# Performance work log

Measured on AMD Instinct MI355X. Metric: run time of the kernel, lower is better.

The kernel has to match this reference:

```python
import jax, jax.numpy as jnp
import numpy as np

B, L, H, NH, E, M, P, NL, BLK = 4, 1024, 768, 12, 24, 4, 552, 97, 64
NEG = -1e30

def setup_inputs() -> dict:
    key = jax.random.key(0)
    ks = jax.random.split(key, 10)
    sequence_output = jax.random.normal(ks[0], (B, L, H), jnp.float32)
    attention = jax.nn.softmax(jax.random.normal(ks[1], (B, NH, L, L), jnp.float32), axis=-1)
    mention_idx = jax.random.randint(ks[2], (B, E, M), 0, L)
    # first mention of each entity always valid, rest random (ragged mention counts)
    mention_mask = jnp.concatenate(
        [jnp.ones((B, E, 1), jnp.float32),
         (jax.random.uniform(ks[3], (B, E, M - 1)) > 0.4).astype(jnp.float32)], axis=-1)
    hts = jax.random.randint(ks[4], (B, P, 2), 0, E)
    s = 0.02
    Wh = jax.random.normal(ks[5], (H, 2 * H), jnp.float32) * s
    bh = jnp.zeros((H,), jnp.float32)
    Wt = jax.random.normal(ks[6], (H, 2 * H), jnp.float32) * s
    bt = jnp.zeros((H,), jnp.float32)
    Wb = jax.random.normal(ks[7], (NL, H * BLK), jnp.float32) * s
    bb = jnp.zeros((NL,), jnp.float32)
    return {"sequence_output": sequence_output, "attention": attention,
            "mention_mask": mention_mask, "Wh": Wh, "bh": bh, "Wt": Wt, "bt": bt,
            "Wb": Wb, "bb": bb, "mention_idx": mention_idx, "hts": hts}

def reference(sequence_output, attention, mention_mask, Wh, bh, Wt, bt, Wb, bb, mention_idx, hts):
    bix = jnp.arange(B)[:, None, None]
    # gather mention embeddings: [B,E,M,H]
    m_emb = sequence_output[bix, mention_idx]
    mask = mention_mask[..., None]
    # entity embedding: logsumexp over valid mentions
    entity_embs = jax.nn.logsumexp(jnp.where(mask > 0, m_emb, NEG), axis=2)  # [B,E,H]
    # gather mention attention rows: [B,E,M,NH,L]; mean over valid mentions
    m_att = attention[bix, :, mention_idx]
    denom = jnp.sum(mention_mask, axis=-1)[:, :, None, None]
    entity_atts = jnp.sum(m_att * mask[..., None], axis=2) / denom  # [B,E,NH,L]
    b2 = jnp.arange(B)[:, None]
    hs = entity_embs[b2, hts[..., 0]]   # [B,P,H]
    ts = entity_embs[b2, hts[..., 1]]
    h_att = entity_atts[b2, hts[..., 0]]  # [B,P,NH,L]
    t_att = entity_atts[b2, hts[..., 1]]
    ht_att = (h_att * t_att).mean(axis=2)                     # [B,P,L]
    ht_att = ht_att / (ht_att.sum(-1, keepdims=True) + 1e-5)
    rs = jnp.einsum('bld,brl->brd', sequence_output, ht_att)  # [B,P,H]
    zh = jnp.tanh(jnp.concatenate([hs, rs], -1) @ Wh.T + bh)  # [B,P,H]
    zt = jnp.tanh(jnp.concatenate([ts, rs], -1) @ Wt.T + bt)
    b1 = zh.reshape(B, P, H // BLK, BLK)
    b2_ = zt.reshape(B, P, H // BLK, BLK)
    bl = (b1[..., :, None] * b2_[..., None, :]).reshape(B, P, H * BLK)
    logits = bl @ Wb.T + bb                                   # [B,P,NL]
    return logits
```

## Files before the change

kernel.cpp:

```cpp
#include <hip/hip_runtime.h>
#include <math.h>

#define B_   4
#define L_   1024
#define H_   768
#define NH_  12
#define E_   24
#define M_   4
#define P_   552
#define NL_  97
#define H2_  1536
#define HB_  49152
#define R_   2208
#define NEG_ (-1e30f)

#define RT2_  9
#define PR2_  2304
#define S_    48
#define NTIL_ 7
#define KT_   1536

typedef _Float16 h2   __attribute__((ext_vector_type(2)));
typedef _Float16 f16x8 __attribute__((ext_vector_type(8)));
typedef float    f32x4 __attribute__((ext_vector_type(4)));

__device__ inline uint pkh(float lo, float hi) {
    union { __fp16 v __attribute__((ext_vector_type(2))); uint u; } c;
    c.v = __builtin_amdgcn_cvt_pkrtz(lo, hi);
    return c.u;
}
__device__ inline ushort h_rne(float x) {
    union { _Float16 h; ushort u; } c; c.h = (_Float16)x; return c.u;
}
__device__ inline uint h2_rne(float lo, float hi) {
    return (uint)h_rne(lo) | ((uint)h_rne(hi) << 16);
}

#define PKB_ATT 1152
#define PKB_WB  2688
#define PKB_W   576
#define PKB_SEQ 1536
#define PKB_EMB 96
__global__ void k_pack(const float* __restrict__ att, const float* __restrict__ Wb,
                       const float* __restrict__ Wh, const float* __restrict__ Wt,
                       const float* __restrict__ seq,
                       const int* __restrict__ midx, const float* __restrict__ mmask,
                       _Float16* __restrict__ ea, _Float16* __restrict__ WbP,
                       _Float16* __restrict__ WhP, _Float16* __restrict__ WtP,
                       _Float16* __restrict__ seqP, _Float16* __restrict__ ee) {
    int bid = blockIdx.x;
    if (bid < PKB_ATT) {
        int blk = bid;
        int n  = blk % NH_;
        int be = blk / NH_;
        int b  = be / E_;
        int idx[M_]; float msk[M_]; float denom = 0.f;
#pragma unroll
        for (int m = 0; m < M_; ++m) { idx[m] = midx[be*M_+m]; msk[m] = mmask[be*M_+m]; denom += msk[m]; }
        float inv = 1.f / denom;
        const float* abase = att + (size_t)(b*NH_ + n) * L_ * L_;
        int l4 = threadIdx.x * 4;
        float s0 = 0.f, s1 = 0.f, s2 = 0.f, s3 = 0.f;
#pragma unroll
        for (int m = 0; m < M_; ++m) {
            float4 a = *(const float4*)(abase + idx[m]*L_ + l4);
            s0 += msk[m]*a.x; s1 += msk[m]*a.y; s2 += msk[m]*a.z; s3 += msk[m]*a.w;
        }
        *(uint2*)(ea + (((size_t)(be*NH_ + n)) << 10) + l4) =
            make_uint2(pkh(s0*inv, s1*inv), pkh(s2*inv, s3*inv));
        return;
    }
    if (bid < PKB_ATT + PKB_WB) {
        int t = (bid - PKB_ATT)*256 + threadIdx.x;
        int lane = t & 63;
        int nt   = (t >> 6) % NTIL_;
        int kt   = t / (NTIL_*64);
        int n = nt*16 + (lane & 15);
        int k = kt*32 + ((lane >> 4) << 3);
        uint w[4] = {0u,0u,0u,0u};
        if (n < NL_) {
            const float* src = Wb + (size_t)n*HB_ + k;
#pragma unroll
            for (int e = 0; e < 4; ++e) w[e] = h2_rne(src[2*e], src[2*e+1]);
        }
        *(uint4*)(WbP + (size_t)t*8) = make_uint4(w[0],w[1],w[2],w[3]);
        return;
    }
    if (bid < PKB_ATT + PKB_WB + 2*PKB_W) {
        int seg = bid - PKB_ATT - PKB_WB;
        const float* W = (seg < PKB_W) ? Wh : Wt;
        _Float16*   WP = (seg < PKB_W) ? WhP : WtP;
        int t = (seg % PKB_W)*256 + threadIdx.x;
        int lane = t & 63;
        int nt   = (t >> 6) % 48;
        int kt   = t / (48*64);
        int n = nt*16 + (lane & 15);
        int k = kt*32 + ((lane >> 4) << 3);
        const float* src = W + (size_t)n*H2_ + k;
        uint w[4];
#pragma unroll
        for (int e = 0; e < 4; ++e) w[e] = h2_rne(src[2*e], src[2*e+1]);
        *(uint4*)(WP + (size_t)t*8) = make_uint4(w[0],w[1],w[2],w[3]);
        return;
    }
    if (bid < PKB_ATT + PKB_WB + 2*PKB_W + PKB_SEQ) {
        int t = (bid - PKB_ATT - PKB_WB - 2*PKB_W)*256 + threadIdx.x;
        int lane = t & 63;
        int rest = t >> 6;
        int nt = rest % 48; rest /= 48;
        int kt = rest % 32;
        int b  = rest / 32;
        int n = nt*16 + (lane & 15);
        int k = kt*32 + ((lane >> 4) << 3);
        const float* src = seq + ((size_t)(b*L_ + k))*H_ + n;
        uint w[4];
#pragma unroll
        for (int e = 0; e < 4; ++e) w[e] = h2_rne(src[(2*e)*H_], src[(2*e+1)*H_]);
        *(uint4*)(seqP + (size_t)t*8) = make_uint4(w[0],w[1],w[2],w[3]);
        return;
    }
    int be = bid - (PKB_ATT + PKB_WB + 2*PKB_W + PKB_SEQ);
    int b  = be / E_;
    int idx[M_]; float msk[M_];
#pragma unroll
    for (int m = 0; m < M_; ++m) { idx[m] = midx[be*M_+m]; msk[m] = mmask[be*M_+m]; }
    for (int d = threadIdx.x; d < H_; d += 256) {
        float v[M_]; float mx = NEG_;
#pragma unroll
        for (int m = 0; m < M_; ++m) {
            v[m] = (msk[m] > 0.f) ? seq[(b*L_ + idx[m])*H_ + d] : NEG_;
            mx = fmaxf(mx, v[m]);
        }
        float s = 0.f;
#pragma unroll
        for (int m = 0; m < M_; ++m) s += expf(v[m] - mx);
        ee[be*H_ + d] = (_Float16)(mx + logf(s));
    }
}

__global__ void k_ht_att(const _Float16* __restrict__ ea, const int* __restrict__ hts,
                         _Float16* __restrict__ ht) {
    __shared__ float red[2];
    int bp = blockIdx.x;
    int b  = bp / P_;
    int h = hts[bp*2+0], t = hts[bp*2+1];
    const uint4* eh4 = (const uint4*)(ea + ((size_t)(b*E_ + h)*NH_ << 10));
    const uint4* et4 = (const uint4*)(ea + ((size_t)(b*E_ + t)*NH_ << 10));
    int lp = threadIdx.x;
    float s[8] = {};
#pragma unroll
    for (int n = 0; n < NH_; ++n) {
        union { uint4 u; h2 v[4]; } A, C;
        A.u = eh4[n*128 + lp];
        C.u = et4[n*128 + lp];
#pragma unroll
        for (int q = 0; q < 4; ++q) {
            s[2*q]   += (float)A.v[q][0]*(float)C.v[q][0];
            s[2*q+1] += (float)A.v[q][1]*(float)C.v[q][1];
        }
    }
    float local = 0.f;
#pragma unroll
    for (int q = 0; q < 8; ++q) { s[q] *= (1.f/NH_); local += s[q]; }
#pragma unroll
    for (int o = 32; o > 0; o >>= 1) local += __shfl_down(local, o);
    int wid = threadIdx.x >> 6, lane = threadIdx.x & 63;
    if (lane == 0) red[wid] = local;
    __syncthreads();
    if (threadIdx.x == 0) red[0] = 1.f / (red[0] + red[1] + 1e-5f);
    __syncthreads();
    float inv = red[0];
    *(uint4*)(ht + ((size_t)bp << 10) + lp*8) =
        make_uint4(pkh(s[0]*inv, s[1]*inv), pkh(s[2]*inv, s[3]*inv),
                   pkh(s[4]*inv, s[5]*inv), pkh(s[6]*inv, s[7]*inv));
}

__launch_bounds__(256, 2)
__global__ void k_rs_mfma(const _Float16* __restrict__ ht, const _Float16* __restrict__ seqP,
                          _Float16* __restrict__ rs) {
    __shared__ _Float16 as[128*72];
    int bid = blockIdx.x;
    int xcd = bid & 7, jj0 = bid >> 3;
    int b    = xcd >> 1;
    int tile = (xcd & 1)*30 + jj0;
    int p0   = (tile % 5) * 128;
    int nt0  = (tile / 5) * 4;
    int wave = threadIdx.x >> 6, lane = threadIdx.x & 63;

    const _Float16* srcp[4];
    int ldst[4];
#pragma unroll
    for (int i = 0; i < 4; ++i) {
        int t = threadIdx.x + i*256;
        int row = t >> 3, c8 = (t & 7)*8;
        int p = p0 + row;
        srcp[i] = (p < P_) ? ht + (((size_t)(b*P_ + p)) << 10) + c8 : nullptr;
        ldst[i] = row*72 + c8;
    }
    uint4 st[4];
#pragma unroll
    for (int i = 0; i < 4; ++i)
        st[i] = srcp[i] ? *(const uint4*)(srcp[i]) : make_uint4(0,0,0,0);

    f32x4 acc[2][4] = {};
    const _Float16* wbase = seqP + ((size_t)b*32*48 + nt0)*512 + lane*8;
    int rowbase = wave*32 + (lane & 15);
    int asub = (lane >> 4) << 3;

    for (int kc = 0; kc < 16; ++kc) {
        if (kc) __syncthreads();
#pragma unroll
        for (int i = 0; i < 4; ++i) *(uint4*)(as + ldst[i]) = st[i];
        __syncthreads();
        if (kc + 1 < 16) {
#pragma unroll
            for (int i = 0; i < 4; ++i)
                st[i] = srcp[i] ? *(const uint4*)(srcp[i] + (kc+1)*64) : make_uint4(0,0,0,0);
        }
#pragma unroll
        for (int kk = 0; kk < 2; ++kk) {
            int kt = kc*2 + kk;
            const _Float16* wp = wbase + (size_t)kt*(48*512);
            f16x8 bf[4];
#pragma unroll
            for (int jn = 0; jn < 4; ++jn) bf[jn] = *(const f16x8*)(wp + jn*512);
#pragma unroll
            for (int ms = 0; ms < 2; ++ms) {
                f16x8 af = *(const f16x8*)(as + (rowbase + ms*16)*72 + kk*32 + asub);
#pragma unroll
                for (int jn = 0; jn < 4; ++jn)
                    acc[ms][jn] = __builtin_amdgcn_mfma_f32_16x16x32_f16(af, bf[jn], acc[ms][jn], 0, 0, 0);
            }
        }
    }
    int crow = (lane >> 4) * 4;
    int ccol = lane & 15;
#pragma unroll
    for (int ms = 0; ms < 2; ++ms) {
#pragma unroll
        for (int jn = 0; jn < 4; ++jn) {
            int n = nt0*16 + jn*16 + ccol;
#pragma unroll
            for (int reg = 0; reg < 4; ++reg) {
                int p = p0 + wave*32 + ms*16 + crow + reg;
                if (p < P_) rs[(size_t)(b*P_ + p)*H_ + n] = (_Float16)acc[ms][jn][reg];
            }
        }
    }
}

__launch_bounds__(256, 2)
__global__ void k_z_mfma(const _Float16* __restrict__ ee, const _Float16* __restrict__ rs,
                         const _Float16* __restrict__ WhP, const _Float16* __restrict__ WtP,
                         const float* __restrict__ bh, const float* __restrict__ bt,
                         const int* __restrict__ hts,
                         _Float16* __restrict__ zh, _Float16* __restrict__ zt) {
    __shared__ _Float16 as[128*72];
    int bid = blockIdx.x;
    int xcd = bid & 7, jj0 = bid >> 3;
    int which = xcd >> 2;
    int tile  = (xcd & 3)*54 + jj0;
    int r0  = (tile % 18) * 128;
    int nt0 = (tile / 18) * 4;
    const _Float16* WP   = which ? WtP : WhP;
    const float*    bias = which ? bt  : bh;
    _Float16*       out  = which ? zt  : zh;
    int wave = threadIdx.x >> 6, lane = threadIdx.x & 63;

    const _Float16* srcA[4];
    const _Float16* srcB[4];
    int ldst[4];
#pragma unroll
    for (int i = 0; i < 4; ++i) {
        int t = threadIdx.x + i*256;
        int row = t >> 3, c8 = (t & 7)*8;
        int r = r0 + row;
        if (r < R_) {
            int b = r / P_;
            int eidx = hts[r*2 + which];
            srcA[i] = ee + (size_t)(b*E_ + eidx)*H_ + c8;
            srcB[i] = rs + (size_t)r*H_ + c8;
        } else { srcA[i] = nullptr; srcB[i] = nullptr; }
        ldst[i] = row*72 + c8;
    }
    uint4 st[4];
#pragma unroll
    for (int i = 0; i < 4; ++i)
        st[i] = srcA[i] ? *(const uint4*)(srcA[i]) : make_uint4(0,0,0,0);

    f32x4 acc[2][4] = {};
    const _Float16* wbase = WP + (size_t)nt0*512 + lane*8;
    int rowbase = wave*32 + (lane & 15);
    int asub = (lane >> 4) << 3;

    for (int kc = 0; kc < 24; ++kc) {
        if (kc) __syncthreads();
#pragma unroll
        for (int i = 0; i < 4; ++i) *(uint4*)(as + ldst[i]) = st[i];
        __syncthreads();
        if (kc + 1 < 24) {
            int kn = kc + 1;
#pragma unroll
            for (int i = 0; i < 4; ++i) {
                const _Float16* s = (kn < 12) ? (srcA[i] ? srcA[i] + kn*64 : nullptr)
                                              : (srcB[i] ? srcB[i] + (kn-12)*64 : nullptr);
                st[i] = s ? *(const uint4*)s : make_uint4(0,0,0,0);
            }
        }
#pragma unroll
        for (int kk = 0; kk < 2; ++kk) {
            int kt = kc*2 + kk;
            const _Float16* wp = wbase + (size_t)kt*(48*512);
            f16x8 bf[4];
#pragma unroll
            for (int jn = 0; jn < 4; ++jn) bf[jn] = *(const f16x8*)(wp + jn*512);
#pragma unroll
            for (int ms = 0; ms < 2; ++ms) {
                f16x8 af = *(const f16x8*)(as + (rowbase + ms*16)*72 + kk*32 + asub);
#pragma unroll
                for (int jn = 0; jn < 4; ++jn)
                    acc[ms][jn] = __builtin_amdgcn_mfma_f32_16x16x32_f16(af, bf[jn], acc[ms][jn], 0, 0, 0);
            }
        }
    }
    int crow = (lane >> 4) * 4;
    int ccol = lane & 15;
#pragma unroll
    for (int ms = 0; ms < 2; ++ms) {
#pragma unroll
        for (int jn = 0; jn < 4; ++jn) {
            int n = nt0*16 + jn*16 + ccol;
            float bv = bias[n];
#pragma unroll
            for (int reg = 0; reg < 4; ++reg) {
                int r = r0 + wave*32 + ms*16 + crow + reg;
                if (r < R_) out[(size_t)r*H_ + n] = (_Float16)tanhf(acc[ms][jn][reg] + bv);
            }
        }
    }
}

__launch_bounds__(256, 2)
__global__ void k_logits_mfma(const _Float16* __restrict__ zh, const _Float16* __restrict__ zt,
                              const _Float16* __restrict__ WbP, _Float16* __restrict__ part) {
    __shared__ _Float16 zhs[256*20];
    __shared__ _Float16 zts[256*72];
    int bid = blockIdx.x;
    int xcd = bid & 7, j = bid >> 3;
    int kc  = xcd*6 + j/9;
    int rt  = j % 9;
    int r0  = rt * 256;
    int g64 = (kc >> 2) * 64;
    int a0  = (kc & 3) * 16;

    for (int it = 0; it < 2; ++it) {
        int t = threadIdx.x + it*256;
        int row = t >> 1, i8 = (t & 1)*8;
        int r = r0 + row;
        uint4 w = make_uint4(0,0,0,0);
        if (r < R_) w = *(const uint4*)(zh + (size_t)r*H_ + g64 + a0 + i8);
        *(uint4*)(zhs + row*20 + i8) = w;
    }
    for (int it = 0; it < 8; ++it) {
        int t = threadIdx.x + it*256;
        int row = t >> 3, j8 = (t & 7)*8;
        int r = r0 + row;
        uint4 w = make_uint4(0,0,0,0);
        if (r < R_) w = *(const uint4*)(zt + (size_t)r*H_ + g64 + j8);
        *(uint4*)(zts + row*72 + j8) = w;
    }
    __syncthreads();

    int wave = threadIdx.x >> 6, lane = threadIdx.x & 63;
    int rowA0 = wave*64 + (lane & 15);
    int jsub  = (lane >> 4) * 8;

    f32x4 acc[4][NTIL_] = {};
    const _Float16* wb0 = WbP + (size_t)(kc*32) * (NTIL_*512) + lane*8;

    f16x8 bf[NTIL_];
#pragma unroll
    for (int nt = 0; nt < NTIL_; ++nt) bf[nt] = *(const f16x8*)(wb0 + nt*512);

    for (int ktl = 0; ktl < 32; ++ktl) {
        f16x8 bn[NTIL_];
        if (ktl + 1 < 32) {
            const _Float16* wp = wb0 + (size_t)(ktl+1) * (NTIL_*512);
#pragma unroll
            for (int nt = 0; nt < NTIL_; ++nt) bn[nt] = *(const f16x8*)(wp + nt*512);
        }
        int il = ktl >> 1;
        int jb = (ktl & 1) * 32 + jsub;
#pragma unroll
        for (int ms = 0; ms < 4; ++ms) {
            int row = rowA0 + ms*16;
            _Float16 hv = zhs[row*20 + il];
            h2 hb = {hv, hv};
            union { uint4 u; h2 v[4]; } T;
            T.u = *(const uint4*)(zts + row*72 + jb);
            union { h2 v[4]; f16x8 f; } A;
            A.v[0] = hb * T.v[0];
            A.v[1] = hb * T.v[1];
            A.v[2] = hb * T.v[2];
            A.v[3] = hb * T.v[3];
#pragma unroll
            for (int nt = 0; nt < NTIL_; ++nt)
                acc[ms][nt] = __builtin_amdgcn_mfma_f32_16x16x32_f16(A.f, bf[nt], acc[ms][nt], 0, 0, 0);
        }
        if (ktl + 1 < 32) {
#pragma unroll
            for (int nt = 0; nt < NTIL_; ++nt) bf[nt] = bn[nt];
        }
    }

    int crow0 = wave*64 + (lane >> 4) * 4;
    int ccol  = lane & 15;
#pragma unroll
    for (int ms = 0; ms < 4; ++ms) {
#pragma unroll
        for (int nt = 0; nt < NTIL_; ++nt) {
#pragma unroll
            for (int reg = 0; reg < 4; ++reg) {
                int rp = r0 + crow0 + ms*16 + reg;
                part[((size_t)kc*PR2_ + rp)*112 + nt*16 + ccol] = (_Float16)acc[ms][nt][reg];
            }
        }
    }
}

__global__ void k_logits_reduce(const _Float16* __restrict__ part, const float* __restrict__ bb,
                                float* __restrict__ out) {
    int idx = blockIdx.x*256 + threadIdx.x;
    if (idx >= R_*NL_) return;
    int r = idx / NL_, n = idx - r*NL_;
    float s = bb[n];
#pragma unroll
    for (int kc = 0; kc < S_; ++kc) s += (float)part[((size_t)kc*PR2_ + r)*112 + n];
    out[idx] = s;
}

extern "C" void kernel_launch(void* const* d_in, const int* in_sizes, int n_in,
                              void* d_out, int out_size, void* d_ws, size_t ws_size,
                              hipStream_t stream) {
    const float* seq   = (const float*)d_in[0];
    const float* att   = (const float*)d_in[1];
    const float* mmask = (const float*)d_in[2];
    const float* Wh    = (const float*)d_in[3];
    const float* bh    = (const float*)d_in[4];
    const float* Wt    = (const float*)d_in[5];
    const float* bt    = (const float*)d_in[6];
    const float* Wb    = (const float*)d_in[7];
    const float* bb    = (const float*)d_in[8];
    const int*   midx  = (const int*)d_in[9];
    const int*   hts   = (const int*)d_in[10];
    float* out = (float*)d_out;

    char* base = (char*)d_ws;
    _Float16* WbP  = (_Float16*)base;  base += (size_t)KT_*NTIL_*64*8 * 2;
    _Float16* WhP  = (_Float16*)base;  base += (size_t)48*48*64*8 * 2;
    _Float16* WtP  = (_Float16*)base;  base += (size_t)48*48*64*8 * 2;
    _Float16* seqP = (_Float16*)base;  base += (size_t)B_*32*48*64*8 * 2;
    _Float16* ee   = (_Float16*)base;  base += (size_t)B_*E_*H_ * 2;
    _Float16* ea   = (_Float16*)base;  base += (size_t)B_*E_*NH_*L_ * 2;
    _Float16* ht   = (_Float16*)base;  base += (size_t)R_*L_ * 2;
    _Float16* rs   = (_Float16*)base;  base += (size_t)R_*H_ * 2;
    _Float16* zh   = (_Float16*)base;  base += (size_t)R_*H_ * 2;
    _Float16* zt   = (_Float16*)base;  base += (size_t)R_*H_ * 2;
    _Float16* part = (_Float16*)base;

    k_pack<<<dim3(PKB_ATT + PKB_WB + 2*PKB_W + PKB_SEQ + PKB_EMB), dim3(256), 0, stream>>>(
        att, Wb, Wh, Wt, seq, midx, mmask, ea, WbP, WhP, WtP, seqP, ee);

    k_ht_att<<<dim3(R_), dim3(128), 0, stream>>>(ea, hts, ht);

    k_rs_mfma<<<dim3(240), dim3(256), 0, stream>>>(ht, seqP, rs);

    k_z_mfma<<<dim3(432), dim3(256), 0, stream>>>(ee, rs, WhP, WtP, bh, bt, hts, zh, zt);

    k_logits_mfma  <<<dim3(432), dim3(256), 0, stream>>>(zh, zt, WbP, part);
    k_logits_reduce<<<dim3((R_*NL_ + 255)/256), dim3(256), 0, stream>>>(part, bb, out);
}
```

Measured before the change: 114.6 us.

## Stage weight packing through LDS with coalesced float4 loads; raise MFMA launch bounds

Weight packing for Wb, Wh and Wt now reads 16-row by 512-column fp32 tiles with coalesced float4 loads into shared memory, then emits the MFMA-fragment fp16 layout from LDS. The old version did strided scalar reads per lane. This is meant to cut uncoalesced global traffic in the pack kernel, which has to read the large Wb matrix. It adds a 33KB LDS array to every k_pack block, including the attention and seq branches that never use it, which may lower occupancy there. The launch bounds of the rs and z MFMA kernels are also raised to 4 blocks per CU, which may force register spills.

```diff
diff --git a/kernel.cpp b/kernel.cpp
--- a/kernel.cpp
+++ b/kernel.cpp
@@ -37,10 +37,12 @@
 }
 
 #define PKB_ATT 1152
-#define PKB_WB  2688
-#define PKB_W   576
+#define PKB_WB2 672
+#define PKB_W2  288
 #define PKB_SEQ 1536
 #define PKB_EMB 96
+#define LDSTR   516
+
 __global__ void k_pack(const float* __restrict__ att, const float* __restrict__ Wb,
                        const float* __restrict__ Wh, const float* __restrict__ Wt,
                        const float* __restrict__ seq,
@@ -48,6 +50,7 @@
                        _Float16* __restrict__ ea, _Float16* __restrict__ WbP,
                        _Float16* __restrict__ WhP, _Float16* __restrict__ WtP,
                        _Float16* __restrict__ seqP, _Float16* __restrict__ ee) {
+    __shared__ float lds[16][LDSTR];
     int bid = blockIdx.x;
     if (bid < PKB_ATT) {
         int blk = bid;
@@ -70,41 +73,49 @@
             make_uint2(pkh(s0*inv, s1*inv), pkh(s2*inv, s3*inv));
         return;
     }
-    if (bid < PKB_ATT + PKB_WB) {
-        int t = (bid - PKB_ATT)*256 + threadIdx.x;
-        int lane = t & 63;
-        int nt   = (t >> 6) % NTIL_;
-        int kt   = t / (NTIL_*64);
-        int n = nt*16 + (lane & 15);
-        int k = kt*32 + ((lane >> 4) << 3);
-        uint w[4] = {0u,0u,0u,0u};
-        if (n < NL_) {
-            const float* src = Wb + (size_t)n*HB_ + k;
-#pragma unroll
-            for (int e = 0; e < 4; ++e) w[e] = h2_rne(src[2*e], src[2*e+1]);
-        }
-        *(uint4*)(WbP + (size_t)t*8) = make_uint4(w[0],w[1],w[2],w[3]);
+    if (bid < PKB_ATT + PKB_WB2 + PKB_W2) {
+        int seg = bid - PKB_ATT;
+        const float* W; _Float16* WP; int nt, kb, N16, Nvalid, Kdim;
+        if (seg < PKB_WB2) {
+            W = Wb; WP = WbP; N16 = 7; Nvalid = NL_; Kdim = HB_;
+            nt = seg % 7; kb = seg / 7;
+        } else {
+            int s2 = seg - PKB_WB2;
+            int which = s2 / 144;
+            int s = s2 % 144;
+            W = which ? Wt : Wh; WP = which ? WtP : WhP;
+            N16 = 48; Nvalid = H_; Kdim = H2_;
+            nt = s % 48; kb = s / 48;
+        }
+        int k0 = kb * 512;
+#pragma unroll
+        for (int it = 0; it < 8; ++it) {
+            int f4 = threadIdx.x + it*256;
+            int row = f4 >> 7;
+            int c4  = (f4 & 127) << 2;
+            int n   = nt*16 + row;
+            float4 v = make_float4(0.f,0.f,0.f,0.f);
+            if (n < Nvalid) v = *(const float4*)(W + (size_t)n*Kdim + k0 + c4);
+            *(float4*)&lds[row][c4] = v;
+        }
+        __syncthreads();
+        int kt0 = kb * 16;
+#pragma unroll
+        for (int it = 0; it < 4; ++it) {
+            int fi = threadIdx.x + it*256;
+            int kt_l = fi >> 6, lane = fi & 63;
+            int n_l = lane & 15;
+            int k_l = kt_l*32 + ((lane >> 4) << 3);
+            float4 a = *(const float4*)&lds[n_l][k_l];
+            float4 b = *(const float4*)&lds[n_l][k_l + 4];
+            uint4 w = make_uint4(h2_rne(a.x,a.y), h2_rne(a.z,a.w),
+                                 h2_rne(b.x,b.y), h2_rne(b.z,b.w));
+            *(uint4*)(WP + (((size_t)(kt0 + kt_l)*N16 + nt) << 9) + lane*8) = w;
+        }
         return;
     }
-    if (bid < PKB_ATT + PKB_WB + 2*PKB_W) {
-        int seg = bid - PKB_ATT - PKB_WB;
-        const float* W = (seg < PKB_W) ? Wh : Wt;
-        _Float16*   WP = (seg < PKB_W) ? WhP : WtP;
-        int t = (seg % PKB_W)*256 + threadIdx.x;
-        int lane = t & 63;
-        int nt   = (t >> 6) % 48;
-        int kt   = t / (48*64);
-        int n = nt*16 + (lane & 15);
-        int k = kt*32 + ((lane >> 4) << 3);
-        const float* src = W + (size_t)n*H2_ + k;
-        uint w[4];
-#pragma unroll
-        for (int e = 0; e < 4; ++e) w[e] = h2_rne(src[2*e], src[2*e+1]);
-        *(uint4*)(WP + (size_t)t*8) = make_uint4(w[0],w[1],w[2],w[3]);
-        return;
-    }
-    if (bid < PKB_ATT + PKB_WB + 2*PKB_W + PKB_SEQ) {
-        int t = (bid - PKB_ATT - PKB_WB - 2*PKB_W)*256 + threadIdx.x;
+    if (bid < PKB_ATT + PKB_WB2 + PKB_W2 + PKB_SEQ) {
+        int t = (bid - PKB_ATT - PKB_WB2 - PKB_W2)*256 + threadIdx.x;
         int lane = t & 63;
         int rest = t >> 6;
         int nt = rest % 48; rest /= 48;
@@ -119,7 +130,7 @@
         *(uint4*)(seqP + (size_t)t*8) = make_uint4(w[0],w[1],w[2],w[3]);
         return;
     }
-    int be = bid - (PKB_ATT + PKB_WB + 2*PKB_W + PKB_SEQ);
+    int be = bid - (PKB_ATT + PKB_WB2 + PKB_W2 + PKB_SEQ);
     int b  = be / E_;
     int idx[M_]; float msk[M_];
 #pragma unroll
@@ -175,7 +186,7 @@
                    pkh(s[4]*inv, s[5]*inv), pkh(s[6]*inv, s[7]*inv));
 }
 
-__launch_bounds__(256, 2)
+__launch_bounds__(256, 4)
 __global__ void k_rs_mfma(const _Float16* __restrict__ ht, const _Float16* __restrict__ seqP,
                           _Float16* __restrict__ rs) {
     __shared__ _Float16 as[128*72];
@@ -249,7 +260,7 @@
     }
 }
 
-__launch_bounds__(256, 2)
+__launch_bounds__(256, 4)
 __global__ void k_z_mfma(const _Float16* __restrict__ ee, const _Float16* __restrict__ rs,
                          const _Float16* __restrict__ WhP, const _Float16* __restrict__ WtP,
                          const float* __restrict__ bh, const float* __restrict__ bt,
@@ -468,7 +479,7 @@
     _Float16* zt   = (_Float16*)base;  base += (size_t)R_*H_ * 2;
     _Float16* part = (_Float16*)base;
 
-    k_pack<<<dim3(PKB_ATT + PKB_WB + 2*PKB_W + PKB_SEQ + PKB_EMB), dim3(256), 0, stream>>>(
+    k_pack<<<dim3(PKB_ATT + PKB_WB2 + PKB_W2 + PKB_SEQ + PKB_EMB), dim3(256), 0, stream>>>(
         att, Wb, Wh, Wt, seq, midx, mmask, ea, WbP, WhP, WtP, seqP, ee);
 
     k_ht_att<<<dim3(R_), dim3(128), 0, stream>>>(ea, hts, ht);
```

Result: no change. 115.0 us (+0.3%).

## Fuse head and tail projections in z kernel to share rs tile loads

Applied to the files above, without the earlier changes.

The z-projection kernel now computes both zh and zt in one block. Each block loads the rs half of the concatenated input once and feeds it to both the Wh and Wt MFMA streams, while keeping separate LDS tiles for the head and tail entity embeddings during the first half of K. The launch changes from 432 blocks of 256 threads to 216 blocks of 512, with each wave covering 16 rows instead of 32. This halves the rs global and LDS traffic, at the cost of fewer blocks, more registers per thread, and each wave loading weight fragments from both weight matrices.

```diff
diff --git a/kernel.cpp b/kernel.cpp
--- a/kernel.cpp
+++ b/kernel.cpp
@@ -50,9 +50,8 @@
                        _Float16* __restrict__ seqP, _Float16* __restrict__ ee) {
     int bid = blockIdx.x;
     if (bid < PKB_ATT) {
-        int blk = bid;
-        int n  = blk % NH_;
-        int be = blk / NH_;
+        int n  = bid % NH_;
+        int be = bid / NH_;
         int b  = be / E_;
         int idx[M_]; float msk[M_]; float denom = 0.f;
 #pragma unroll
@@ -249,92 +248,110 @@
     }
 }
 
-__launch_bounds__(256, 2)
+__launch_bounds__(512, 2)
 __global__ void k_z_mfma(const _Float16* __restrict__ ee, const _Float16* __restrict__ rs,
                          const _Float16* __restrict__ WhP, const _Float16* __restrict__ WtP,
                          const float* __restrict__ bh, const float* __restrict__ bt,
                          const int* __restrict__ hts,
                          _Float16* __restrict__ zh, _Float16* __restrict__ zt) {
-    __shared__ _Float16 as[128*72];
+    __shared__ _Float16 as0[128*72];
+    __shared__ _Float16 as1[128*72];
     int bid = blockIdx.x;
-    int xcd = bid & 7, jj0 = bid >> 3;
-    int which = xcd >> 2;
-    int tile  = (xcd & 3)*54 + jj0;
+    int xcd = bid & 7, j = bid >> 3;
+    int tile = xcd*27 + j;
     int r0  = (tile % 18) * 128;
     int nt0 = (tile / 18) * 4;
-    const _Float16* WP   = which ? WtP : WhP;
-    const float*    bias = which ? bt  : bh;
-    _Float16*       out  = which ? zt  : zh;
-    int wave = threadIdx.x >> 6, lane = threadIdx.x & 63;
-
-    const _Float16* srcA[4];
-    const _Float16* srcB[4];
-    int ldst[4];
-#pragma unroll
-    for (int i = 0; i < 4; ++i) {
-        int t = threadIdx.x + i*256;
+    int tid = threadIdx.x;
+    int wave = tid >> 6, lane = tid & 63;
+
+    const _Float16* srcA0[2];
+    const _Float16* srcA1[2];
+    const _Float16* srcB[2];
+    int ldst[2];
+#pragma unroll
+    for (int i = 0; i < 2; ++i) {
+        int t = tid + i*512;
         int row = t >> 3, c8 = (t & 7)*8;
         int r = r0 + row;
         if (r < R_) {
             int b = r / P_;
-            int eidx = hts[r*2 + which];
-            srcA[i] = ee + (size_t)(b*E_ + eidx)*H_ + c8;
-            srcB[i] = rs + (size_t)r*H_ + c8;
-        } else { srcA[i] = nullptr; srcB[i] = nullptr; }
+            int e0 = hts[r*2+0], e1 = hts[r*2+1];
+            srcA0[i] = ee + (size_t)(b*E_ + e0)*H_ + c8;
+            srcA1[i] = ee + (size_t)(b*E_ + e1)*H_ + c8;
+            srcB[i]  = rs + (size_t)r*H_ + c8;
+        } else { srcA0[i] = nullptr; srcA1[i] = nullptr; srcB[i] = nullptr; }
         ldst[i] = row*72 + c8;
     }
-    uint4 st[4];
-#pragma unroll
-    for (int i = 0; i < 4; ++i)
-        st[i] = srcA[i] ? *(const uint4*)(srcA[i]) : make_uint4(0,0,0,0);
-
-    f32x4 acc[2][4] = {};
-    const _Float16* wbase = WP + (size_t)nt0*512 + lane*8;
-    int rowbase = wave*32 + (lane & 15);
+    uint4 st0[2], st1[2];
+#pragma unroll
+    for (int i = 0; i < 2; ++i) {
+        st0[i] = srcA0[i] ? *(const uint4*)(srcA0[i]) : make_uint4(0,0,0,0);
+        st1[i] = srcA1[i] ? *(const uint4*)(srcA1[i]) : make_uint4(0,0,0,0);
+    }
+
+    f32x4 acc0[4] = {};
+    f32x4 acc1[4] = {};
+    const _Float16* wbH = WhP + (size_t)nt0*512 + lane*8;
+    const _Float16* wbT = WtP + (size_t)nt0*512 + lane*8;
+    int rowA = wave*16 + (lane & 15);
     int asub = (lane >> 4) << 3;
 
     for (int kc = 0; kc < 24; ++kc) {
         if (kc) __syncthreads();
-#pragma unroll
-        for (int i = 0; i < 4; ++i) *(uint4*)(as + ldst[i]) = st[i];
+        bool dual = (kc < 12);
+#pragma unroll
+        for (int i = 0; i < 2; ++i) *(uint4*)(as0 + ldst[i]) = st0[i];
+        if (dual) {
+#pragma unroll
+            for (int i = 0; i < 2; ++i) *(uint4*)(as1 + ldst[i]) = st1[i];
+        }
         __syncthreads();
-        if (kc + 1 < 24) {
-            int kn = kc + 1;
-#pragma unroll
-            for (int i = 0; i < 4; ++i) {
-                const _Float16* s = (kn < 12) ? (srcA[i] ? srcA[i] + kn*64 : nullptr)
-                                              : (srcB[i] ? srcB[i] + (kn-12)*64 : nullptr);
-                st[i] = s ? *(const uint4*)s : make_uint4(0,0,0,0);
+        int kn = kc + 1;
+        if (kn < 24) {
+            if (kn < 12) {
+#pragma unroll
+                for (int i = 0; i < 2; ++i) {
+                    st0[i] = srcA0[i] ? *(const uint4*)(srcA0[i] + kn*64) : make_uint4(0,0,0,0);
+                    st1[i] = srcA1[i] ? *(const uint4*)(srcA1[i] + kn*64) : make_uint4(0,0,0,0);
+                }
+            } else {
+#pragma unroll
+                for (int i = 0; i < 2; ++i)
+                    st0[i] = srcB[i] ? *(const uint4*)(srcB[i] + (kn-12)*64) : make_uint4(0,0,0,0);
             }
         }
 #pragma unroll
         for (int kk = 0; kk < 2; ++kk) {
             int kt = kc*2 + kk;
-            const _Float16* wp = wbase + (size_t)kt*(48*512);
-            f16x8 bf[4];
-#pragma unroll
-            for (int jn = 0; jn < 4; ++jn) bf[jn] = *(const f16x8*)(wp + jn*512);
-#pragma unroll
-            for (int ms = 0; ms < 2; ++ms) {
-                f16x8 af = *(const f16x8*)(as + (rowbase + ms*16)*72 + kk*32 + asub);
-#pragma unroll
-                for (int jn = 0; jn < 4; ++jn)
-                    acc[ms][jn] = __builtin_amdgcn_mfma_f32_16x16x32_f16(af, bf[jn], acc[ms][jn], 0, 0, 0);
+            const _Float16* wpH = wbH + (size_t)kt*(48*512);
+            const _Float16* wpT = wbT + (size_t)kt*(48*512);
+            f16x8 bfH[4], bfT[4];
+#pragma unroll
+            for (int jn = 0; jn < 4; ++jn) {
+                bfH[jn] = *(const f16x8*)(wpH + jn*512);
+                bfT[jn] = *(const f16x8*)(wpT + jn*512);
+            }
+            f16x8 af0 = *(const f16x8*)(as0 + rowA*72 + kk*32 + asub);
+            f16x8 af1 = dual ? *(const f16x8*)(as1 + rowA*72 + kk*32 + asub) : af0;
+#pragma unroll
+            for (int jn = 0; jn < 4; ++jn) {
+                acc0[jn] = __builtin_amdgcn_mfma_f32_16x16x32_f16(af0, bfH[jn], acc0[jn], 0, 0, 0);
+                acc1[jn] = __builtin_amdgcn_mfma_f32_16x16x32_f16(af1, bfT[jn], acc1[jn], 0, 0, 0);
             }
         }
     }
     int crow = (lane >> 4) * 4;
     int ccol = lane & 15;
 #pragma unroll
-    for (int ms = 0; ms < 2; ++ms) {
-#pragma unroll
-        for (int jn = 0; jn < 4; ++jn) {
-            int n = nt0*16 + jn*16 + ccol;
-            float bv = bias[n];
-#pragma unroll
-            for (int reg = 0; reg < 4; ++reg) {
-                int r = r0 + wave*32 + ms*16 + crow + reg;
-                if (r < R_) out[(size_t)r*H_ + n] = (_Float16)tanhf(acc[ms][jn][reg] + bv);
+    for (int jn = 0; jn < 4; ++jn) {
+        int n = nt0*16 + jn*16 + ccol;
+        float bvh = bh[n], bvt = bt[n];
+#pragma unroll
+        for (int reg = 0; reg < 4; ++reg) {
+            int r = r0 + wave*16 + crow + reg;
+            if (r < R_) {
+                zh[(size_t)r*H_ + n] = (_Float16)tanhf(acc0[jn][reg] + bvh);
+                zt[(size_t)r*H_ + n] = (_Float16)tanhf(acc1[jn][reg] + bvt);
             }
         }
     }
@@ -475,7 +492,7 @@
 
     k_rs_mfma<<<dim3(240), dim3(256), 0, stream>>>(ht, seqP, rs);
 
-    k_z_mfma<<<dim3(432), dim3(256), 0, stream>>>(ee, rs, WhP, WtP, bh, bt, hts, zh, zt);
+    k_z_mfma<<<dim3(216), dim3(512), 0, stream>>>(ee, rs, WhP, WtP, bh, bt, hts, zh, zt);
 
     k_logits_mfma  <<<dim3(432), dim3(256), 0, stream>>>(zh, zt, WbP, part);
     k_logits_reduce<<<dim3((R_*NL_ + 255)/256), dim3(256), 0, stream>>>(part, bb, out);
```

New measurement: 120.2 us. 1.05x slower.
